# Kernel tuning notes

Measured on AMD Instinct MI355X. Metric: run time of the kernel, lower is better.

Reference implementation:

```python
import jax, jax.numpy as jnp
import numpy as np

DIM = 768
HEAD = 12
DK = DIM // HEAD

def setup_inputs() -> dict:
    key = jax.random.key(0)
    ks = jax.random.split(key, 9)
    B, L = 4, 2048
    s = 1.0 / np.sqrt(DIM)
    qkv = jax.random.normal(ks[0], (B, L, DIM), dtype=jnp.float32)
    mask = jnp.ones((B, L), dtype=jnp.int32)
    Wq = jax.random.normal(ks[1], (DIM, DIM), dtype=jnp.float32) * s
    bq = jnp.zeros((DIM,), dtype=jnp.float32)
    Wk = jax.random.normal(ks[2], (DIM, DIM), dtype=jnp.float32) * s
    bk = jnp.zeros((DIM,), dtype=jnp.float32)
    Wv = jax.random.normal(ks[3], (DIM, DIM), dtype=jnp.float32) * s
    bv = jnp.zeros((DIM,), dtype=jnp.float32)
    Wo = jax.random.normal(ks[4], (DIM, DIM), dtype=jnp.float32) * s
    bo = jnp.zeros((DIM,), dtype=jnp.float32)
    return {"qkv": qkv, "mask": mask, "Wq": Wq, "bq": bq, "Wk": Wk, "bk": bk,
            "Wv": Wv, "bv": bv, "Wo": Wo, "bo": bo}

def reference(qkv, mask, Wq, bq, Wk, bk, Wv, bv, Wo, bo):
    B, L, _ = qkv.shape
    def proj(W, b):
        # [B,L,dim] -> [B,H,L,dk]
        return (qkv @ W + b).reshape(B, L, HEAD, DK).transpose(0, 2, 1, 3)
    q, k, v = proj(Wq, bq), proj(Wk, bk), proj(Wv, bv)
    scores = jnp.einsum('bhqd,bhkd->bhqk', q, k) / jnp.sqrt(jnp.float32(DK))
    # mask: [B,L] broadcast over heads and query positions (key axis)
    m = mask[:, None, None, :]  # [B,1,1,L]
    scores = jnp.where(m == 0, jnp.float32(-1e9), scores)
    p = jax.nn.softmax(scores, axis=-1)
    x = jnp.einsum('bhqk,bhkd->bhqd', p, v)  # [B,H,L,dk]
    x = x.transpose(0, 2, 1, 3).reshape(B, L, DIM)
    return x @ Wo + bo
```

## Files before the change

kernel.cpp:

```cpp
#include <hip/hip_runtime.h>
#include <hip/hip_bf16.h>
#include <stdint.h>

#define DIM  768
#define NHEAD 12
#define DK   64
#define BATCH 4
#define SEQ  2048
#define ROWS (BATCH*SEQ)
#define SCL  0.1803368801111204f

typedef __bf16 bf16_t;
typedef bf16_t bf16x8 __attribute__((ext_vector_type(8)));
typedef bf16_t bf16x4 __attribute__((ext_vector_type(4)));
typedef float  f32x4  __attribute__((ext_vector_type(4)));
typedef float  f32x16 __attribute__((ext_vector_type(16)));

typedef unsigned int __attribute__((address_space(1)))* as1p;
typedef unsigned int __attribute__((address_space(3)))* as3p;

__device__ __forceinline__ void gload_lds16(const void* g, void* l) {
    __builtin_amdgcn_global_load_lds((as1p)g, (as3p)l, 16, 0, 0);
}
#define MEMFENCE asm volatile("" ::: "memory")

__global__ void cast_bf16_kernel(const float* __restrict__ in, bf16_t* __restrict__ out) {
    int i = blockIdx.x * 256 + threadIdx.x;
    const float4* p = (const float4*)in;
    float4 a = p[(size_t)i*2], b = p[(size_t)i*2+1];
    bf16x8 v;
    v[0]=(bf16_t)a.x; v[1]=(bf16_t)a.y; v[2]=(bf16_t)a.z; v[3]=(bf16_t)a.w;
    v[4]=(bf16_t)b.x; v[5]=(bf16_t)b.y; v[6]=(bf16_t)b.z; v[7]=(bf16_t)b.w;
    *(bf16x8*)(out + (size_t)i*8) = v;
}

__global__ void wtrans_kernel(const float* __restrict__ W0, const float* __restrict__ W1,
                              const float* __restrict__ W2, const float* __restrict__ W3,
                              bf16_t* __restrict__ T0, bf16_t* __restrict__ T1,
                              bf16_t* __restrict__ T2, bf16_t* __restrict__ T3) {
    const float* W = blockIdx.z==0?W0 : blockIdx.z==1?W1 : blockIdx.z==2?W2 : W3;
    bf16_t*      T = blockIdx.z==0?T0 : blockIdx.z==1?T1 : blockIdx.z==2?T2 : T3;
    __shared__ float tile[32][33];
    int tx = threadIdx.x, ty = threadIdx.y;
    int c = blockIdx.x*32 + tx;
    #pragma unroll
    for (int r = 0; r < 32; r += 8)
        tile[ty+r][tx] = W[(size_t)(blockIdx.y*32 + ty + r)*DIM + c];
    __syncthreads();
    int oc = blockIdx.y*32 + tx;
    #pragma unroll
    for (int r = 0; r < 32; r += 8)
        T[(size_t)(blockIdx.x*32 + ty + r)*DIM + oc] = (bf16_t)tile[tx][ty+r];
}

template<int MODE>
__global__ __launch_bounds__(256) void gemm_kernel(
    const bf16_t* __restrict__ A,
    const bf16_t* __restrict__ WTa, const bf16_t* __restrict__ WTb, const bf16_t* __restrict__ WTc,
    const float* __restrict__ ba, const float* __restrict__ bb, const float* __restrict__ bc,
    bf16_t* __restrict__ Qo, bf16_t* __restrict__ Ko, bf16_t* __restrict__ Vo,
    float* __restrict__ Oo) {
    __shared__ __align__(16) bf16_t As[2][128*64];
    __shared__ __align__(16) bf16_t Bs[2][128*64];
    const int tid = threadIdx.x, wave = tid>>6, lane = tid&63;
    const int wm = wave>>1, wn = wave&1;
    const int b = blockIdx.x;
    const int xcd = b & 7, ib = b >> 3;
    int z, ntile, mtile;
    if (MODE == 0) { z = ib % 3; ntile = (ib/3) % 6; mtile = xcd*8 + ib/18; }
    else           { z = 0;      ntile = ib % 6;     mtile = xcd*8 + ib/6;  }
    const int m0 = mtile*128, n0 = ntile*128;
    const bf16_t* WT  = (z==0) ? WTa : (z==1 ? WTb : WTc);
    const float* bias = (z==0) ? ba  : (z==1 ? bb  : bc);

    f32x4 acc[4][4];
    const f32x4 zf = {0.f,0.f,0.f,0.f};
    #pragma unroll
    for (int m = 0; m < 4; ++m)
        #pragma unroll
        for (int n = 0; n < 4; ++n) acc[m][n] = zf;

    const int srow = wave*32 + (lane>>3);
    const int scol = (lane&7)*8;
    const bf16_t* Ag = A  + (size_t)(m0+srow)*DIM + scol;
    const bf16_t* Bg = WT + (size_t)(n0+srow)*DIM + scol;
    const int woff = (wave*32)*64;

    #pragma unroll
    for (int i2 = 0; i2 < 4; ++i2) {
        gload_lds16(Ag + (size_t)(i2*8)*DIM, &As[0][woff + i2*8*64]);
        gload_lds16(Bg + (size_t)(i2*8)*DIM, &Bs[0][woff + i2*8*64]);
    }

    int cur = 0;
    for (int t = 0; t < DIM/64; ++t) {
        if (t < DIM/64 - 1) {
            const size_t k1 = (size_t)(t+1)*64;
            #pragma unroll
            for (int i2 = 0; i2 < 4; ++i2) {
                gload_lds16(Ag + (size_t)(i2*8)*DIM + k1, &As[cur^1][woff + i2*8*64]);
                gload_lds16(Bg + (size_t)(i2*8)*DIM + k1, &Bs[cur^1][woff + i2*8*64]);
            }
            asm volatile("s_waitcnt vmcnt(8)" ::: "memory");
        } else {
            asm volatile("s_waitcnt vmcnt(0)" ::: "memory");
        }
        MEMFENCE; __builtin_amdgcn_s_barrier(); MEMFENCE;

        #pragma unroll
        for (int ks = 0; ks < 2; ++ks) {
            bf16x8 af[4], bfr[4];
            #pragma unroll
            for (int m = 0; m < 4; ++m)
                af[m]  = *(const bf16x8*)&As[cur][(wm*64 + m*16 + (lane&15))*64 + ks*32 + (lane>>4)*8];
            #pragma unroll
            for (int n = 0; n < 4; ++n)
                bfr[n] = *(const bf16x8*)&Bs[cur][(wn*64 + n*16 + (lane&15))*64 + ks*32 + (lane>>4)*8];
            #pragma unroll
            for (int m = 0; m < 4; ++m)
                #pragma unroll
                for (int n = 0; n < 4; ++n)
                    acc[m][n] = __builtin_amdgcn_mfma_f32_16x16x32_bf16(af[m], bfr[n], acc[m][n], 0, 0, 0);
        }
        MEMFENCE; __builtin_amdgcn_s_barrier(); MEMFENCE;
        cur ^= 1;
    }

    float bvv[4];
    #pragma unroll
    for (int n = 0; n < 4; ++n) bvv[n] = bias[n0 + wn*64 + n*16 + (lane&15)];

    #pragma unroll
    for (int m = 0; m < 4; ++m) {
        #pragma unroll
        for (int n = 0; n < 4; ++n) {
            #pragma unroll
            for (int r = 0; r < 4; ++r) {
                float val = acc[m][n][r] + bvv[n];
                int R = m0 + wm*64 + m*16 + (lane>>4)*4 + r;
                int C = n0 + wn*64 + n*16 + (lane&15);
                if (MODE == 1) {
                    Oo[(size_t)R*DIM + C] = val;
                } else {
                    int bi = R>>11, li = R&2047, h = C>>6, d = C&63;
                    size_t bh = (size_t)(bi*NHEAD + h);
                    if      (z==0) Qo[(bh*SEQ + li)*DK + d] = (bf16_t)(val*SCL);
                    else if (z==1) Ko[(bh*SEQ + li)*DK + d] = (bf16_t)val;
                    else {
                        int li2 = (li & ~12) | ((li&4)<<1) | ((li&8)>>1);
                        Vo[(bh*DK + d)*SEQ + li2] = (bf16_t)val;
                    }
                }
            }
        }
    }
}

#define NT (SEQ/64)

__global__ __launch_bounds__(256) void attn_kernel(
    const bf16_t* __restrict__ Q, const bf16_t* __restrict__ K, const bf16_t* __restrict__ VT,
    const int* __restrict__ mask, bf16_t* __restrict__ X) {
    __shared__ __align__(16) bf16_t lds[2*8192];
    const int tid = threadIdx.x, wv = tid>>6, lane = tid&63;
    const int lo5 = lane&31, hi5 = lane>>5;
    const int b = blockIdx.x;
    const int xcd = b & 7, ii = b >> 3;
    const int bh = xcd*6 + (ii>>4), qt = ii & 15;
    const int bi = bh/NHEAD, h = bh%NHEAD;
    const bf16_t* Qb = Q  + (size_t)bh*SEQ*DK;
    const bf16_t* Kb = K  + (size_t)bh*SEQ*DK;
    const bf16_t* Vb = VT + (size_t)bh*DK*SEQ;
    const int* mk = mask + (size_t)bi*SEQ + lo5;
    const int q0 = qt*128 + wv*32;

    int mOk = 1;
    {
        const int4* m4 = (const int4*)(mask + (size_t)bi*SEQ);
        #pragma unroll
        for (int i2 = 0; i2 < 8; ++i2) {
            int4 v = m4[lane + i2*64];
            mOk &= (v.x != 0) & (v.y != 0) & (v.z != 0) & (v.w != 0);
        }
    }
    const int mAll = __all(mOk);

    bf16x8 qf[4];
    #pragma unroll
    for (int ks = 0; ks < 4; ++ks)
        qf[ks] = *(const bf16x8*)&Qb[(size_t)(q0 + lo5)*DK + ks*16 + hi5*8];

    f32x16 O0, O1;
    #pragma unroll
    for (int r = 0; r < 16; ++r) { O0[r] = 0.f; O1[r] = 0.f; }
    float lsum = 0.f;

    bf16x8 onesb = {};
    if (hi5 == 0) onesb[0] = (bf16_t)1.0f;

    const int srow  = wv*16 + (lane>>3);
    const int sslot = (lane&7) ^ (srow&7);
    const bf16_t* Kg = Kb + (size_t)srow*DK  + sslot*8;
    const bf16_t* Vg = Vb + (size_t)srow*SEQ + sslot*8;
    int koff[4];
    #pragma unroll
    for (int ks = 0; ks < 4; ++ks) koff[ks] = (((2*ks + hi5) ^ (lo5 & 7)) << 3);

    #pragma unroll
    for (int i = 0; i < 2; ++i) {
        gload_lds16(Kg + (size_t)(i*8)*DK,  lds +        (wv*16 + i*8)*64);
        gload_lds16(Vg + (size_t)(i*8)*SEQ, lds + 4096 + (wv*16 + i*8)*64);
    }

    int cur = 0;
    for (int t = 0; t < NT; ++t) {
        const int kv0 = t*64;
        if (t < NT-1) {
            bf16_t* nb = lds + (cur^1)*8192;
            #pragma unroll
            for (int i = 0; i < 2; ++i) {
                gload_lds16(Kg + (size_t)(kv0+64)*DK + (size_t)(i*8)*DK,  nb +        (wv*16 + i*8)*64);
                gload_lds16(Vg + (kv0+64)            + (size_t)(i*8)*SEQ, nb + 4096 + (wv*16 + i*8)*64);
            }
            asm volatile("s_waitcnt vmcnt(4)" ::: "memory");
        } else {
            asm volatile("s_waitcnt vmcnt(0)" ::: "memory");
        }
        MEMFENCE; __builtin_amdgcn_s_barrier(); MEMFENCE;

        const bf16_t* Kt = lds + cur*8192;
        const bf16_t* Vt = lds + cur*8192 + 4096;

        f32x16 s0, s1;
        #pragma unroll
        for (int r = 0; r < 16; ++r) { s0[r] = -12.f; s1[r] = -12.f; }
        #pragma unroll
        for (int ks = 0; ks < 4; ++ks) {
            bf16x8 a0 = *(const bf16x8*)&Kt[ lo5     *64 + koff[ks]];
            bf16x8 a1 = *(const bf16x8*)&Kt[(32+lo5)*64 + koff[ks]];
            s0 = __builtin_amdgcn_mfma_f32_32x32x16_bf16(a0, qf[ks], s0, 0, 0, 0);
            s1 = __builtin_amdgcn_mfma_f32_32x32x16_bf16(a1, qf[ks], s1, 0, 0, 0);
        }
        if (!mAll) {
            int mv0 = mk[kv0], mv1 = mk[kv0 + 32];
            bf16x8 ba = {};
            ba[0] = mv0 ? (bf16_t)0.f : (bf16_t)(-1024.0f);
            s0 = __builtin_amdgcn_mfma_f32_32x32x16_bf16(ba, onesb, s0, 0, 0, 0);
            ba[0] = mv1 ? (bf16_t)0.f : (bf16_t)(-1024.0f);
            s1 = __builtin_amdgcn_mfma_f32_32x32x16_bf16(ba, onesb, s1, 0, 0, 0);
        }

        #pragma unroll
        for (int r = 0; r < 16; ++r) {
            s0[r] = __builtin_amdgcn_exp2f(s0[r]);
            s1[r] = __builtin_amdgcn_exp2f(s1[r]);
        }
        float t01[16];
        #pragma unroll
        for (int r = 0; r < 16; ++r) t01[r] = s0[r] + s1[r];
        float u[8];
        #pragma unroll
        for (int r = 0; r < 8; ++r) u[r] = t01[r] + t01[r+8];
        float w0 = (u[0]+u[1]) + (u[2]+u[3]);
        float w1 = (u[4]+u[5]) + (u[6]+u[7]);
        float ps = w0 + w1;
        lsum += ps + __shfl_xor(ps, 32);

        bf16x8 pf0, pf1, pf2, pf3;
        #pragma unroll
        for (int j = 0; j < 8; ++j) {
            pf0[j] = (bf16_t)s0[j];
            pf1[j] = (bf16_t)s0[8+j];
            pf2[j] = (bf16_t)s1[j];
            pf3[j] = (bf16_t)s1[8+j];
        }

        #pragma unroll
        for (int ks = 0; ks < 4; ++ks) {
            bf16x8 pb = (ks==0) ? pf0 : (ks==1) ? pf1 : (ks==2) ? pf2 : pf3;
            bf16x8 a0 = *(const bf16x8*)&Vt[ lo5     *64 + koff[ks]];
            bf16x8 a1 = *(const bf16x8*)&Vt[(32+lo5)*64 + koff[ks]];
            O0 = __builtin_amdgcn_mfma_f32_32x32x16_bf16(a0, pb, O0, 0, 0, 0);
            O1 = __builtin_amdgcn_mfma_f32_32x32x16_bf16(a1, pb, O1, 0, 0, 0);
        }
        MEMFENCE; __builtin_amdgcn_s_barrier(); MEMFENCE;
        cur ^= 1;
    }

    float rl = __builtin_amdgcn_rcpf(lsum);
    const size_t rowb = (size_t)(bi*SEQ + q0 + lo5)*DIM + h*DK;
    #pragma unroll
    for (int g = 0; g < 4; ++g) {
        bf16x4 v0, v1;
        #pragma unroll
        for (int j = 0; j < 4; ++j) {
            v0[j] = (bf16_t)(O0[g*4+j] * rl);
            v1[j] = (bf16_t)(O1[g*4+j] * rl);
        }
        *(bf16x4*)&X[rowb + g*8 + hi5*4]      = v0;
        *(bf16x4*)&X[rowb + 32 + g*8 + hi5*4] = v1;
    }
}

extern "C" void kernel_launch(void* const* d_in, const int* in_sizes, int n_in,
                              void* d_out, int out_size, void* d_ws, size_t ws_size,
                              hipStream_t stream) {
    (void)in_sizes; (void)n_in; (void)out_size; (void)ws_size;
    const float* qkv = (const float*)d_in[0];
    const int*  mask = (const int*)d_in[1];
    const float* Wq = (const float*)d_in[2];
    const float* bq = (const float*)d_in[3];
    const float* Wk = (const float*)d_in[4];
    const float* bk = (const float*)d_in[5];
    const float* Wv = (const float*)d_in[6];
    const float* bv = (const float*)d_in[7];
    const float* Wo = (const float*)d_in[8];
    const float* bo = (const float*)d_in[9];
    float* out = (float*)d_out;

    char* ws = (char*)d_ws;
    size_t off = 0;
    auto carve = [&](size_t bytes) { void* p = ws + off; off += (bytes + 255) & ~(size_t)255; return p; };
    const size_t actN = (size_t)ROWS*DIM;
    bf16_t* Abf = (bf16_t*)carve(actN*2);
    bf16_t* WTq = (bf16_t*)carve((size_t)DIM*DIM*2);
    bf16_t* WTk = (bf16_t*)carve((size_t)DIM*DIM*2);
    bf16_t* WTv = (bf16_t*)carve((size_t)DIM*DIM*2);
    bf16_t* WTo = (bf16_t*)carve((size_t)DIM*DIM*2);
    bf16_t* Qb  = (bf16_t*)carve(actN*2);
    bf16_t* Kb  = (bf16_t*)carve(actN*2);
    bf16_t* VTb = (bf16_t*)carve(actN*2);
    bf16_t* Xb  = (bf16_t*)carve(actN*2);

    cast_bf16_kernel<<<dim3(ROWS*DIM/8/256), dim3(256), 0, stream>>>(qkv, Abf);
    wtrans_kernel<<<dim3(24,24,4), dim3(32,8), 0, stream>>>(Wq, Wk, Wv, Wo, WTq, WTk, WTv, WTo);
    gemm_kernel<0><<<dim3(1152), dim3(256), 0, stream>>>(Abf, WTq, WTk, WTv, bq, bk, bv,
                                                         Qb, Kb, VTb, nullptr);
    attn_kernel<<<dim3(768), dim3(256), 0, stream>>>(Qb, Kb, VTb, mask, Xb);
    gemm_kernel<1><<<dim3(384), dim3(256), 0, stream>>>(Xb, WTo, WTo, WTo, bo, bo, bo,
                                                        nullptr, nullptr, nullptr, out);
}
```

Before: 168.8 us.

## Fuse Q/K/V projections into one GEMM kernel sharing the A tile

Adds a dedicated QKV projection kernel where each block loads one activation tile and three weight tiles per k-step and accumulates Q, K and V together. This removes the threefold reload of the activation tile across separate blocks. In exchange it uses a single LDS buffer (no double buffering), triples accumulator registers, and launches a third as many blocks, which reduces occupancy and parallelism.

```diff
diff --git a/kernel.cpp b/kernel.cpp
--- a/kernel.cpp
+++ b/kernel.cpp
@@ -51,6 +51,116 @@
     #pragma unroll
     for (int r = 0; r < 32; r += 8)
         T[(size_t)(blockIdx.x*32 + ty + r)*DIM + oc] = (bf16_t)tile[tx][ty+r];
+}
+
+__global__ __launch_bounds__(256) void gemmqkv_kernel(
+    const bf16_t* __restrict__ A,
+    const bf16_t* __restrict__ WTq, const bf16_t* __restrict__ WTk, const bf16_t* __restrict__ WTv,
+    const float* __restrict__ bq, const float* __restrict__ bk, const float* __restrict__ bv,
+    bf16_t* __restrict__ Qo, bf16_t* __restrict__ Ko, bf16_t* __restrict__ Vo) {
+    __shared__ __align__(16) bf16_t As[128*64];
+    __shared__ __align__(16) bf16_t Bs[3][128*64];
+    const int tid = threadIdx.x, wave = tid>>6, lane = tid&63;
+    const int wm = wave>>1, wn = wave&1;
+    const int b = blockIdx.x;
+    const int xcd = b & 7, ib = b >> 3;
+    const int mtile = xcd*8 + ib/6, ntile = ib % 6;
+    const int m0 = mtile*128, n0 = ntile*128;
+
+    f32x4 accQ[4][4], accK[4][4], accV[4][4];
+    const f32x4 zf = {0.f,0.f,0.f,0.f};
+    #pragma unroll
+    for (int m = 0; m < 4; ++m)
+        #pragma unroll
+        for (int n = 0; n < 4; ++n) { accQ[m][n] = zf; accK[m][n] = zf; accV[m][n] = zf; }
+
+    const int srow = wave*32 + (lane>>3);
+    const int scol = (lane&7)*8;
+    const bf16_t* Ag  = A   + (size_t)(m0+srow)*DIM + scol;
+    const bf16_t* Bgq = WTq + (size_t)(n0+srow)*DIM + scol;
+    const bf16_t* Bgk = WTk + (size_t)(n0+srow)*DIM + scol;
+    const bf16_t* Bgv = WTv + (size_t)(n0+srow)*DIM + scol;
+    const int woff = (wave*32)*64;
+
+    for (int t = 0; t < DIM/64; ++t) {
+        const size_t k0 = (size_t)t*64;
+        MEMFENCE; __builtin_amdgcn_s_barrier(); MEMFENCE;
+        #pragma unroll
+        for (int i2 = 0; i2 < 4; ++i2) {
+            gload_lds16(Ag  + (size_t)(i2*8)*DIM + k0, &As[woff + i2*8*64]);
+            gload_lds16(Bgq + (size_t)(i2*8)*DIM + k0, &Bs[0][woff + i2*8*64]);
+            gload_lds16(Bgk + (size_t)(i2*8)*DIM + k0, &Bs[1][woff + i2*8*64]);
+            gload_lds16(Bgv + (size_t)(i2*8)*DIM + k0, &Bs[2][woff + i2*8*64]);
+        }
+        asm volatile("s_waitcnt vmcnt(0)" ::: "memory");
+        MEMFENCE; __builtin_amdgcn_s_barrier(); MEMFENCE;
+
+        #pragma unroll
+        for (int ks = 0; ks < 2; ++ks) {
+            bf16x8 af[4];
+            #pragma unroll
+            for (int m = 0; m < 4; ++m)
+                af[m] = *(const bf16x8*)&As[(wm*64 + m*16 + (lane&15))*64 + ks*32 + (lane>>4)*8];
+            {
+                bf16x8 bfr[4];
+                #pragma unroll
+                for (int n = 0; n < 4; ++n)
+                    bfr[n] = *(const bf16x8*)&Bs[0][(wn*64 + n*16 + (lane&15))*64 + ks*32 + (lane>>4)*8];
+                #pragma unroll
+                for (int m = 0; m < 4; ++m)
+                    #pragma unroll
+                    for (int n = 0; n < 4; ++n)
+                        accQ[m][n] = __builtin_amdgcn_mfma_f32_16x16x32_bf16(af[m], bfr[n], accQ[m][n], 0, 0, 0);
+            }
+            {
+                bf16x8 bfr[4];
+                #pragma unroll
+                for (int n = 0; n < 4; ++n)
+                    bfr[n] = *(const bf16x8*)&Bs[1][(wn*64 + n*16 + (lane&15))*64 + ks*32 + (lane>>4)*8];
+                #pragma unroll
+                for (int m = 0; m < 4; ++m)
+                    #pragma unroll
+                    for (int n = 0; n < 4; ++n)
+                        accK[m][n] = __builtin_amdgcn_mfma_f32_16x16x32_bf16(af[m], bfr[n], accK[m][n], 0, 0, 0);
+            }
+            {
+                bf16x8 bfr[4];
+                #pragma unroll
+                for (int n = 0; n < 4; ++n)
+                    bfr[n] = *(const bf16x8*)&Bs[2][(wn*64 + n*16 + (lane&15))*64 + ks*32 + (lane>>4)*8];
+                #pragma unroll
+                for (int m = 0; m < 4; ++m)
+                    #pragma unroll
+                    for (int n = 0; n < 4; ++n)
+                        accV[m][n] = __builtin_amdgcn_mfma_f32_16x16x32_bf16(af[m], bfr[n], accV[m][n], 0, 0, 0);
+            }
+        }
+    }
+
+    float bvQ[4], bvK[4], bvV[4];
+    #pragma unroll
+    for (int n = 0; n < 4; ++n) {
+        int c = n0 + wn*64 + n*16 + (lane&15);
+        bvQ[n] = bq[c]; bvK[n] = bk[c]; bvV[n] = bv[c];
+    }
+
+    #pragma unroll
+    for (int m = 0; m < 4; ++m) {
+        #pragma unroll
+        for (int n = 0; n < 4; ++n) {
+            #pragma unroll
+            for (int r = 0; r < 4; ++r) {
+                int R = m0 + wm*64 + m*16 + (lane>>4)*4 + r;
+                int C = n0 + wn*64 + n*16 + (lane&15);
+                int bi = R>>11, li = R&2047, h = C>>6, d = C&63;
+                size_t bh = (size_t)(bi*NHEAD + h);
+                Qo[(bh*SEQ + li)*DK + d] = (bf16_t)((accQ[m][n][r] + bvQ[n])*SCL);
+                Ko[(bh*SEQ + li)*DK + d] = (bf16_t)(accK[m][n][r] + bvK[n]);
+                int li2 = (li & ~12) | ((li&4)<<1) | ((li&8)>>1);
+                Vo[(bh*DK + d)*SEQ + li2] = (bf16_t)(accV[m][n][r] + bvV[n]);
+            }
+        }
+    }
 }
 
 template<int MODE>
@@ -334,8 +444,8 @@
 
     cast_bf16_kernel<<<dim3(ROWS*DIM/8/256), dim3(256), 0, stream>>>(qkv, Abf);
     wtrans_kernel<<<dim3(24,24,4), dim3(32,8), 0, stream>>>(Wq, Wk, Wv, Wo, WTq, WTk, WTv, WTo);
-    gemm_kernel<0><<<dim3(1152), dim3(256), 0, stream>>>(Abf, WTq, WTk, WTv, bq, bk, bv,
-                                                         Qb, Kb, VTb, nullptr);
+    gemmqkv_kernel<<<dim3(384), dim3(256), 0, stream>>>(Abf, WTq, WTk, WTv, bq, bk, bv,
+                                                        Qb, Kb, VTb);
     attn_kernel<<<dim3(768), dim3(256), 0, stream>>>(Qb, Kb, VTb, mask, Xb);
     gemm_kernel<1><<<dim3(384), dim3(256), 0, stream>>>(Xb, WTo, WTo, WTo, bo, bo, bo,
                                                         nullptr, nullptr, nullptr, out);
```

Measured after the change: 172.8 us. 1.02x slower.
